# Kernel optimization log

Hardware: AMD Instinct MI355X
Metric: run time of the kernel (lower is better)

Reference implementation:

```python
import jax, jax.numpy as jnp
import numpy as np

B, T, D = 4, 2048, 2048
H, G, HD = 16, 4, 128
NB, BS = 512, 16  # num_blocks, block_size
GS = H // G
SCALE = HD ** -0.5
NEG = -1e30


def setup_inputs() -> dict:
    key = jax.random.key(0)
    ks = jax.random.split(key, 5)
    x = jax.random.normal(ks[0], (B, T, D), dtype=jnp.float32)
    block_tables = jnp.arange(B * (T // BS), dtype=jnp.int32).reshape(B, T // BS)
    kv_lens = jnp.zeros((B,), dtype=jnp.int32)
    k_blocks = jnp.zeros((NB, G, BS, HD), jnp.float32)
    v_blocks = jnp.zeros((NB, G, BS, HD), jnp.float32)
    w_q = jax.random.normal(ks[1], (D, H * HD), jnp.float32) * 0.02
    w_k = jax.random.normal(ks[2], (D, G * HD), jnp.float32) * 0.02
    w_v = jax.random.normal(ks[3], (D, G * HD), jnp.float32) * 0.02
    w_o = jax.random.normal(ks[4], (H * HD, D), jnp.float32) * 0.02
    return {"x": x, "w_q": w_q, "w_k": w_k, "w_v": w_v, "w_o": w_o,
            "k_blocks": k_blocks, "v_blocks": v_blocks,
            "block_tables": block_tables, "kv_lens": kv_lens}


def reference(x, w_q, w_k, w_v, w_o, k_blocks, v_blocks, block_tables, kv_lens):
    # projections
    q = (x @ w_q).reshape(B, T, H, HD).transpose(0, 2, 1, 3)   # [B,H,T,Hd]
    k = (x @ w_k).reshape(B, T, G, HD).transpose(0, 2, 1, 3)   # [B,G,T,Hd]
    v = (x @ w_v).reshape(B, T, G, HD).transpose(0, 2, 1, 3)

    # paged cache append (vectorized scatter over [B,T])
    pos = kv_lens[:, None] + jnp.arange(T)                     # [B,T]
    slot, off = pos // BS, pos % BS
    bid = jnp.take_along_axis(block_tables, slot, axis=1)      # [B,T] block ids
    k_blocks = k_blocks.at[bid, :, off, :].set(k.transpose(0, 2, 1, 3))
    v_blocks = v_blocks.at[bid, :, off, :].set(v.transpose(0, 2, 1, 3))

    # gather contiguous KV per request; prefill: kv_lens == 0 -> seq_len = T
    S = T
    nb = (S + BS - 1) // BS
    blk = block_tables[:, :nb]                                 # [B,nb]
    k_seq = k_blocks[blk].transpose(0, 2, 1, 3, 4).reshape(B, G, nb * BS, HD)[:, :, :S]
    v_seq = v_blocks[blk].transpose(0, 2, 1, 3, 4).reshape(B, G, nb * BS, HD)[:, :, :S]

    # original's flat reshapes pair head h with kv group (h % G)
    qg = q.reshape(B, GS, G, T, HD)
    scores = jnp.einsum('bjgqd,bgkd->bjgqk', qg, k_seq) * SCALE

    q_pos = (S - T) + jnp.arange(T)
    k_pos = jnp.arange(S)
    causal = k_pos[None, :] <= q_pos[:, None]                  # [T,S]
    scores = jnp.where(causal, scores, NEG)
    attn = jax.nn.softmax(scores, axis=-1)

    out = jnp.einsum('bjgqk,bgkd->bjgqd', attn, v_seq)         # [B,GS,G,T,Hd]
    out = out.reshape(B, H, T, HD).transpose(0, 2, 1, 3).reshape(B, T, H * HD)
    return out @ w_o
```

## Files before the change

### kernel.cpp

```cpp
#include <hip/hip_runtime.h>
#include <stdint.h>

typedef __attribute__((ext_vector_type(8))) short short8;
typedef __attribute__((ext_vector_type(8))) unsigned short ushort8;
typedef __attribute__((ext_vector_type(4))) float f32x4;

__device__ __forceinline__ ushort f2bf(float f) {
  union { float f; uint32_t u; } v; v.f = f;
  uint32_t r = v.u + 0x7FFFu + ((v.u >> 16) & 1u);
  return (ushort)(r >> 16);
}

__device__ __forceinline__ ushort f2bf_trunc(float f) {
  union { float f; uint32_t u; } v; v.f = f;
  return (ushort)(v.u >> 16);
}

__device__ __forceinline__ float fexp2(float x) {
  float r;
  asm("v_exp_f32 %0, %1" : "=v"(r) : "v"(x));
  return r;
}

__device__ __forceinline__ void gld16(const ushort* g, ushort* l) {
  __builtin_amdgcn_global_load_lds((const __attribute__((address_space(1))) void*)g,
                                   (__attribute__((address_space(3))) void*)l, 16, 0, 0);
}

__global__ __launch_bounds__(256) void k_f32_to_bf16(const float* __restrict__ in,
                                                     ushort* __restrict__ out, long n) {
  long i = ((long)blockIdx.x * 256 + threadIdx.x) * 8;
  if (i >= n) return;
  float4 a = *(const float4*)(in + i);
  float4 b = *(const float4*)(in + i + 4);
  ushort8 o;
  o[0] = f2bf(a.x); o[1] = f2bf(a.y); o[2] = f2bf(a.z); o[3] = f2bf(a.w);
  o[4] = f2bf(b.x); o[5] = f2bf(b.y); o[6] = f2bf(b.z); o[7] = f2bf(b.w);
  *(ushort8*)(out + i) = o;
}

__global__ __launch_bounds__(256) void k_w_transpose(const float* __restrict__ in,
                                                     ushort* __restrict__ out, int R, int C) {
  __shared__ float t[32][33];
  int tx = threadIdx.x & 31, ty = threadIdx.x >> 5;
  int r0 = blockIdx.y * 32, c0 = blockIdx.x * 32;
#pragma unroll
  for (int i = 0; i < 4; i++)
    t[ty + i * 8][tx] = in[(size_t)(r0 + ty + i * 8) * C + c0 + tx];
  __syncthreads();
#pragma unroll
  for (int i = 0; i < 4; i++)
    out[(size_t)(c0 + ty + i * 8) * R + r0 + tx] = f2bf(t[tx][ty + i * 8]);
}

__global__ __launch_bounds__(256) void k_v_transpose(const ushort* __restrict__ qkv,
                                                     ushort* __restrict__ out) {
  __shared__ ushort t[32][33];
  int tx = threadIdx.x & 31, ty = threadIdx.x >> 5;
  int t0 = blockIdx.x * 32, d0 = blockIdx.y * 32;
  int b = blockIdx.z >> 2, g = blockIdx.z & 3;
#pragma unroll
  for (int i = 0; i < 4; i++)
    t[ty + i * 8][tx] =
        qkv[((size_t)b * 2048 + t0 + ty + i * 8) * 3072 + 2560 + g * 128 + d0 + tx];
  __syncthreads();
#pragma unroll
  for (int i = 0; i < 4; i++)
    out[(((size_t)b * 4 + g) * 128 + d0 + ty + i * 8) * 2048 + t0 + tx] = t[tx][ty + i * 8];
}

template <int NCH8>
__device__ __forceinline__ void stageT(const ushort* G, int ldg, ushort* Ls, int tid) {
  int l = tid & 63, w = tid >> 6;
  int rsub = l >> 3;
  int cs = ((l & 7) ^ rsub) << 3;
#pragma unroll
  for (int n = 0; n < NCH8; n++) {
    int c = n * 8 + w;
    gld16(G + (size_t)(c * 8 + rsub) * ldg + cs, Ls + c * 512 + l * 8);
  }
}

template <int F32OUT, int NF>
__global__ __launch_bounds__(512) void k_gemm256(const ushort* __restrict__ A,
                                                 const ushort* __restrict__ BT,
                                                 void* __restrict__ C, int M, int N, int K) {
  constexpr int BN = NF * 64;
  __shared__ ushort As0[256 * 64], As1[256 * 64];
  __shared__ ushort Bs0[BN * 64], Bs1[BN * 64];
  const int tid = threadIdx.x;
  const int lane = tid & 63, wid = tid >> 6;
  const int wm = wid >> 2, wn = wid & 3;
  const int l15 = lane & 15, l4 = lane >> 4;
  const int rsw = (l15 & 7) << 3;
  int nwg = gridDim.x * gridDim.y;
  int lin = blockIdx.y * gridDim.x + blockIdx.x;
  int swz = (lin & 7) * (nwg >> 3) + (lin >> 3);
  int bx = swz % gridDim.x, by = swz / gridDim.x;
  const int m0 = by * 256, n0 = bx * BN;

  const ushort* Atile = A + (size_t)m0 * K;
  const ushort* Btile = BT + (size_t)n0 * K;
  const int NK = K >> 6;

  f32x4 acc[8][NF] = {};

  stageT<4>(Atile, K, As0, tid);
  stageT<NF>(Btile, K, Bs0, tid);
  stageT<4>(Atile + 64, K, As1, tid);
  stageT<NF>(Btile + 64, K, Bs1, tid);
  if constexpr (NF == 4) asm volatile("s_waitcnt vmcnt(8)" ::: "memory");
  else                   asm volatile("s_waitcnt vmcnt(7)" ::: "memory");
  asm volatile("s_barrier" ::: "memory");

  for (int kt = 0; kt < NK; ++kt) {
    const ushort* Ab = (kt & 1) ? As1 : As0;
    const ushort* Bb = (kt & 1) ? Bs1 : Bs0;
    short8 bfrag[NF][2];
#pragma unroll
    for (int nf = 0; nf < NF; nf++)
#pragma unroll
      for (int ks = 0; ks < 2; ks++)
        bfrag[nf][ks] = *(const short8*)&Bb[(wn * (NF * 16) + nf * 16 + l15) * 64 +
                                            ((ks * 32 + l4 * 8) ^ rsw)];
#pragma unroll
    for (int q = 0; q < 4; q++) {
      short8 afr[2][2];
#pragma unroll
      for (int dm = 0; dm < 2; dm++)
#pragma unroll
        for (int ks = 0; ks < 2; ks++)
          afr[dm][ks] = *(const short8*)&Ab[(wm * 128 + (q * 2 + dm) * 16 + l15) * 64 +
                                            ((ks * 32 + l4 * 8) ^ rsw)];
      __builtin_amdgcn_s_setprio(1);
#pragma unroll
      for (int dm = 0; dm < 2; dm++)
#pragma unroll
        for (int nf = 0; nf < NF; nf++)
#pragma unroll
          for (int ks = 0; ks < 2; ks++)
            acc[q * 2 + dm][nf] = __builtin_amdgcn_mfma_f32_16x16x32_bf16(
                afr[dm][ks], bfrag[nf][ks], acc[q * 2 + dm][nf], 0, 0, 0);
      __builtin_amdgcn_s_setprio(0);
    }
    asm volatile("s_barrier" ::: "memory");
    if (kt + 2 < NK) {
      stageT<4>(Atile + (kt + 2) * 64, K, (kt & 1) ? As1 : As0, tid);
      stageT<NF>(Btile + (kt + 2) * 64, K, (kt & 1) ? Bs1 : Bs0, tid);
      if constexpr (NF == 4) asm volatile("s_waitcnt vmcnt(8)" ::: "memory");
      else                   asm volatile("s_waitcnt vmcnt(7)" ::: "memory");
    } else {
      asm volatile("s_waitcnt vmcnt(0)" ::: "memory");
    }
    asm volatile("s_barrier" ::: "memory");
  }

#pragma unroll
  for (int mf = 0; mf < 8; mf++)
#pragma unroll
    for (int nf = 0; nf < NF; nf++)
#pragma unroll
      for (int r = 0; r < 4; r++) {
        int m = m0 + wm * 128 + mf * 16 + l4 * 4 + r;
        int n = n0 + wn * (NF * 16) + nf * 16 + l15;
        if (F32OUT)
          ((float*)C)[(size_t)m * N + n] = acc[mf][nf][r];
        else
          ((ushort*)C)[(size_t)m * N + n] = f2bf(acc[mf][nf][r]);
      }
}

__device__ __forceinline__ void stageA_half(const ushort* Atile, int K, int t,
                                            ushort* slot, int h, int tid) {
#pragma unroll
  for (int n = 0; n < 2; n++) {
    int row = h * 128 + n * 64 + (tid >> 3);
    int c0 = (tid & 7) * 8;
    int cs = c0 ^ ((row & 7) << 3);
    gld16(Atile + (size_t)row * K + t * 64 + cs, slot + row * 64 + c0);
  }
}

__device__ __forceinline__ void stageB_third(const ushort* Btile, int K, int t,
                                             ushort* slot, int b, int tid) {
  int row = b * 64 + (tid >> 3);
  int c0 = (tid & 7) * 8;
  int cs = c0 ^ ((row & 7) << 3);
  gld16(Btile + (size_t)row * K + t * 64 + cs, slot + row * 64 + c0);
}

__global__ __launch_bounds__(512) void k_gemm192p(const ushort* __restrict__ A,
                                                  const ushort* __restrict__ BT,
                                                  ushort* __restrict__ C, int M, int N, int K) {
  __shared__ ushort As[3][16384];
  __shared__ ushort Bs[2][12288];
  const int tid = threadIdx.x;
  const int lane = tid & 63, wid = tid >> 6;
  const int wm = wid >> 2, wn = wid & 3;
  const int l15 = lane & 15, l4 = lane >> 4;
  const int rsw = (l15 & 7) << 3;
  int nwg = gridDim.x * gridDim.y;
  int lin = blockIdx.y * gridDim.x + blockIdx.x;
  int swz = (lin & 7) * (nwg >> 3) + (lin >> 3);
  int bx = swz % gridDim.x, by = swz / gridDim.x;
  const int m0 = by * 256, n0 = bx * 192;
  const ushort* Atile = A + (size_t)m0 * K;
  const ushort* Btile = BT + (size_t)n0 * K;
  const int NK = K >> 6;

  f32x4 acc[8][3] = {};

  stageA_half(Atile, K, 0, As[0], 0, tid);
  stageA_half(Atile, K, 0, As[0], 1, tid);
  stageB_third(Btile, K, 0, Bs[0], 0, tid);
  stageB_third(Btile, K, 0, Bs[0], 1, tid);
  stageB_third(Btile, K, 0, Bs[0], 2, tid);
  stageA_half(Atile, K, 1, As[1], 0, tid);
  stageA_half(Atile, K, 1, As[1], 1, tid);
  stageB_third(Btile, K, 1, Bs[1], 0, tid);
  stageB_third(Btile, K, 1, Bs[1], 1, tid);
  stageB_third(Btile, K, 1, Bs[1], 2, tid);
  asm volatile("s_waitcnt vmcnt(7)" ::: "memory");
  asm volatile("s_barrier" ::: "memory");

#pragma unroll 1
  for (int t = 0; t < NK; ++t) {
    const ushort* Ab = As[t % 3];
    const ushort* Bb = Bs[t & 1];
    ushort* An = As[(t + 2) % 3];
    ushort* Bn = Bs[t & 1];
    const bool st = (t + 2 < NK);
    short8 bfrag[3][2];

#pragma unroll
    for (int nf = 0; nf < 3; nf++)
#pragma unroll
      for (int ks = 0; ks < 2; ks++)
        bfrag[nf][ks] = *(const short8*)&Bb[(wn * 48 + nf * 16 + l15) * 64 +
                                            ((ks * 32 + l4 * 8) ^ rsw)];
    {
      short8 afr[2][2];
#pragma unroll
      for (int dm = 0; dm < 2; dm++)
#pragma unroll
        for (int ks = 0; ks < 2; ks++)
          afr[dm][ks] = *(const short8*)&Ab[(wm * 128 + dm * 16 + l15) * 64 +
                                            ((ks * 32 + l4 * 8) ^ rsw)];
      if (st) stageA_half(Atile, K, t + 2, An, 0, tid);
      asm volatile("s_barrier" ::: "memory");
      __builtin_amdgcn_s_setprio(1);
#pragma unroll
      for (int dm = 0; dm < 2; dm++)
#pragma unroll
        for (int nf = 0; nf < 3; nf++)
#pragma unroll
          for (int ks = 0; ks < 2; ks++)
            acc[dm][nf] = __builtin_amdgcn_mfma_f32_16x16x32_bf16(
                afr[dm][ks], bfrag[nf][ks], acc[dm][nf], 0, 0, 0);
      __builtin_amdgcn_s_setprio(0);
      asm volatile("s_barrier" ::: "memory");
    }
#pragma unroll
    for (int q = 1; q < 4; q++) {
      short8 afr[2][2];
#pragma unroll
      for (int dm = 0; dm < 2; dm++)
#pragma unroll
        for (int ks = 0; ks < 2; ks++)
          afr[dm][ks] = *(const short8*)&Ab[(wm * 128 + (q * 2 + dm) * 16 + l15) * 64 +
                                            ((ks * 32 + l4 * 8) ^ rsw)];
      if (st) {
        if (q == 1) stageB_third(Btile, K, t + 2, Bn, 0, tid);
        if (q == 2) stageB_third(Btile, K, t + 2, Bn, 1, tid);
        if (q == 3) {
          stageA_half(Atile, K, t + 2, An, 1, tid);
          stageB_third(Btile, K, t + 2, Bn, 2, tid);
        }
      }
      asm volatile("s_barrier" ::: "memory");
      __builtin_amdgcn_s_setprio(1);
#pragma unroll
      for (int dm = 0; dm < 2; dm++)
#pragma unroll
        for (int nf = 0; nf < 3; nf++)
#pragma unroll
          for (int ks = 0; ks < 2; ks++)
            acc[q * 2 + dm][nf] = __builtin_amdgcn_mfma_f32_16x16x32_bf16(
                afr[dm][ks], bfrag[nf][ks], acc[q * 2 + dm][nf], 0, 0, 0);
      __builtin_amdgcn_s_setprio(0);
      if (q < 3) {
        asm volatile("s_barrier" ::: "memory");
      } else {
        if (st) asm volatile("s_waitcnt vmcnt(7)" ::: "memory");
        else    asm volatile("s_waitcnt vmcnt(0)" ::: "memory");
        asm volatile("s_barrier" ::: "memory");
      }
    }
  }

#pragma unroll
  for (int mf = 0; mf < 8; mf++)
#pragma unroll
    for (int nf = 0; nf < 3; nf++)
#pragma unroll
      for (int r = 0; r < 4; r++) {
        int m = m0 + wm * 128 + mf * 16 + l4 * 4 + r;
        int n = n0 + wn * 48 + nf * 16 + l15;
        C[(size_t)m * N + n] = f2bf(acc[mf][nf][r]);
      }
}

__device__ __forceinline__ void stage_k8(const ushort* Kt, ushort* Ks, int tid) {
  int l = tid & 63, w = tid >> 6;
#pragma unroll
  for (int n = 0; n < 2; n++) {
    int cidx = w * 2 + n;
    int r = cidx * 4 + (l >> 4);
    int cs = ((l & 15) * 8) ^ ((r & 7) << 3);
    gld16(Kt + (size_t)r * 3072 + cs, Ks + cidx * 512 + l * 8);
  }
}

__device__ __forceinline__ void stage_v8(const ushort* Vt, ushort* Vs, int tid) {
  int l = tid & 63, w = tid >> 6;
#pragma unroll
  for (int n = 0; n < 2; n++) {
    int cidx = w * 2 + n;
    int d = cidx * 8 + (l >> 3);
    int cs = ((l & 7) * 8) ^ ((d & 7) << 3);
    gld16(Vt + (size_t)d * 2048 + cs, Vs + cidx * 512 + l * 8);
  }
}

__global__ __launch_bounds__(512) void k_attn(const ushort* __restrict__ QKV,
                                              const ushort* __restrict__ VT,
                                              ushort* __restrict__ O) {
  const int T = 2048, HD = 128, G = 4, H = 16, RS = 3072;
  const float SCALE2 = 0.08838834764831845f * 1.4426950408889634f;
  const float MFIX = 12.0f;
  int bid = blockIdx.x;
  int pr = bid >> 6;
  int bh = bid & 63;
  int h = bh & 15, b = bh >> 4;
  int g = h & 3;
  int tid = threadIdx.x, wid = tid >> 6, lane = tid & 63;
  int l15 = lane & 15, l4 = lane >> 4;
  int kswz = (l15 & 7) << 3;

  __shared__ __align__(16) char smem[102400];
  ushort* Ks0 = (ushort*)smem;
  ushort* Ks1 = (ushort*)(smem + 16384);
  ushort* Vs0 = (ushort*)(smem + 32768);
  ushort* Vs1 = (ushort*)(smem + 49152);
  ushort* Pw  = (ushort*)(smem + 65536) + wid * (32 * 72);

  const ushort* Qb = &QKV[(size_t)b * T * RS + h * HD];
  const ushort* Kb = &QKV[(size_t)b * T * RS + 2048 + g * HD];
  const ushort* Vb = &VT[((size_t)b * G + g) * (size_t)HD * T];

#pragma unroll 1
  for (int half = 0; half < 2; half++) {
    int ch = half ? pr : (7 - pr);
    int qw = ch * 256 + wid * 32;
    int nt = 4 * (ch + 1);

    short8 qf[2][4];
#pragma unroll
    for (int mf = 0; mf < 2; mf++)
#pragma unroll
      for (int kf = 0; kf < 4; kf++)
        qf[mf][kf] = *(const short8*)&Qb[(size_t)(qw + mf * 16 + l15) * RS + kf * 32 + l4 * 8];

    f32x4 o[2][8] = {};
    float lrow[8];
#pragma unroll
    for (int i = 0; i < 8; i++) lrow[i] = 0.f;

    stage_k8(Kb, Ks0, tid);
    stage_v8(Vb, Vs0, tid);
    __syncthreads();

#pragma unroll 1
    for (int it = 0; it < nt; ++it) {
      int t0 = it * 64;
      int cur = it & 1;
      ushort* Kc = cur ? Ks1 : Ks0;
      ushort* Vc = cur ? Vs1 : Vs0;
      if (it + 1 < nt) {
        stage_k8(Kb + (size_t)(t0 + 64) * RS, cur ? Ks0 : Ks1, tid);
        stage_v8(Vb + t0 + 64, cur ? Vs0 : Vs1, tid);
      }
      if (t0 <= qw + 31) {
        f32x4 s[2][4] = {};
#pragma unroll
        for (int kf = 0; kf < 4; kf++) {
#pragma unroll
          for (int nf = 0; nf < 4; nf++) {
            short8 bk = *(const short8*)&Kc[(nf * 16 + l15) * 128 + ((kf * 32 + l4 * 8) ^ kswz)];
            s[0][nf] = __builtin_amdgcn_mfma_f32_16x16x32_bf16(qf[0][kf], bk, s[0][nf], 0, 0, 0);
            s[1][nf] = __builtin_amdgcn_mfma_f32_16x16x32_bf16(qf[1][kf], bk, s[1][nf], 0, 0, 0);
          }
        }
        bool needmask = (t0 + 63 > qw);
        if (needmask) {
#pragma unroll
          for (int mf = 0; mf < 2; mf++)
#pragma unroll
            for (int nf = 0; nf < 4; nf++)
#pragma unroll
              for (int r = 0; r < 4; r++) {
                int qq = qw + mf * 16 + l4 * 4 + r;
                int kk = t0 + nf * 16 + l15;
                if (kk > qq) s[mf][nf][r] = -1e30f;
              }
        }
        float rs[8];
#pragma unroll
        for (int i = 0; i < 8; i++) rs[i] = 0.f;
#pragma unroll
        for (int mf = 0; mf < 2; mf++)
#pragma unroll
          for (int nf = 0; nf < 4; nf++)
#pragma unroll
            for (int r = 0; r < 4; r++) {
              float pq = fexp2(__builtin_fmaf(s[mf][nf][r], SCALE2, -MFIX));
              rs[mf * 4 + r] += pq;
              Pw[(mf * 16 + l4 * 4 + r) * 72 + nf * 16 + l15] = f2bf_trunc(pq);
            }
#pragma unroll
        for (int i = 0; i < 8; i++) lrow[i] += rs[i];
#pragma unroll
        for (int kf = 0; kf < 2; kf++) {
          short8 pa0 = *(const short8*)&Pw[(l15) * 72 + kf * 32 + l4 * 8];
          short8 pa1 = *(const short8*)&Pw[(16 + l15) * 72 + kf * 32 + l4 * 8];
#pragma unroll
          for (int nfo = 0; nfo < 8; nfo++) {
            short8 bv = *(const short8*)&Vc[(nfo * 16 + l15) * 64 + ((kf * 32 + l4 * 8) ^ kswz)];
            o[0][nfo] = __builtin_amdgcn_mfma_f32_16x16x32_bf16(pa0, bv, o[0][nfo], 0, 0, 0);
            o[1][nfo] = __builtin_amdgcn_mfma_f32_16x16x32_bf16(pa1, bv, o[1][nfo], 0, 0, 0);
          }
        }
      }
      __syncthreads();
    }

#pragma unroll
    for (int i = 0; i < 8; i++) {
      float x = lrow[i];
      x += __shfl_xor(x, 1);
      x += __shfl_xor(x, 2);
      x += __shfl_xor(x, 4);
      x += __shfl_xor(x, 8);
      lrow[i] = x;
    }
    float inv[8];
#pragma unroll
    for (int i = 0; i < 8; i++) inv[i] = 1.0f / lrow[i];
#pragma unroll
    for (int mf = 0; mf < 2; mf++)
#pragma unroll
      for (int nfo = 0; nfo < 8; nfo++)
#pragma unroll
        for (int r = 0; r < 4; r++) {
          int t = qw + mf * 16 + l4 * 4 + r;
          int d = nfo * 16 + l15;
          O[(((size_t)b * T + t) * H + h) * HD + d] = f2bf(o[mf][nfo][r] * inv[mf * 4 + r]);
        }
    __syncthreads();
  }
}

extern "C" void kernel_launch(void* const* d_in, const int* in_sizes, int n_in,
                              void* d_out, int out_size, void* d_ws, size_t ws_size,
                              hipStream_t stream) {
  const float* x   = (const float*)d_in[0];
  const float* w_q = (const float*)d_in[1];
  const float* w_k = (const float*)d_in[2];
  const float* w_v = (const float*)d_in[3];
  const float* w_o = (const float*)d_in[4];

  char* ws = (char*)d_ws;
  ushort* xbf  = (ushort*)(ws);
  ushort* wkvT = (ushort*)(ws + 33554432ul);
  ushort* woT  = (ushort*)(ws + 46137344ul);
  ushort* qkvb = (ushort*)(ws + 54525952ul);
  ushort* VTb  = (ushort*)(ws + 104857600ul);
  ushort* attn = xbf;

  k_f32_to_bf16<<<8192, 256, 0, stream>>>(x, xbf, 16777216L);
  k_w_transpose<<<dim3(64, 64), 256, 0, stream>>>(w_q, wkvT, 2048, 2048);
  k_w_transpose<<<dim3(16, 64), 256, 0, stream>>>(w_k, wkvT + 2048ul * 2048, 2048, 512);
  k_w_transpose<<<dim3(16, 64), 256, 0, stream>>>(w_v, wkvT + 2560ul * 2048, 2048, 512);
  k_w_transpose<<<dim3(64, 64), 256, 0, stream>>>(w_o, woT, 2048, 2048);

  k_gemm192p<<<dim3(16, 32), 512, 0, stream>>>(xbf, wkvT, qkvb, 8192, 3072, 2048);

  k_v_transpose<<<dim3(64, 4, 16), 256, 0, stream>>>(qkvb, VTb);

  k_attn<<<256, 512, 0, stream>>>(qkvb, VTb, attn);

  k_gemm256<1, 4><<<dim3(8, 32), 512, 0, stream>>>(attn, woT, (float*)d_out, 8192, 2048, 2048);
}
```

Baseline: 306.4 us.

## Replace output-projection GEMM with interleaved-staging pipelined 256x256 kernel

The output projection GEMM is switched to a new kernel that triple-buffers A and double-buffers B in shared memory. Global-to-LDS loads for tile t+2 are split into pieces and issued between the four MFMA sub-phases, with barriers around each. This spreads memory traffic across the compute phases instead of issuing it all in one burst after the MFMAs. The cost is more barriers per K step and a larger LDS footprint (160KB), which may limit occupancy.

```diff
diff --git a/kernel.cpp b/kernel.cpp
--- a/kernel.cpp
+++ b/kernel.cpp
@@ -67,107 +67,6 @@
 #pragma unroll
   for (int i = 0; i < 4; i++)
     out[(((size_t)b * 4 + g) * 128 + d0 + ty + i * 8) * 2048 + t0 + tx] = t[tx][ty + i * 8];
-}
-
-template <int NCH8>
-__device__ __forceinline__ void stageT(const ushort* G, int ldg, ushort* Ls, int tid) {
-  int l = tid & 63, w = tid >> 6;
-  int rsub = l >> 3;
-  int cs = ((l & 7) ^ rsub) << 3;
-#pragma unroll
-  for (int n = 0; n < NCH8; n++) {
-    int c = n * 8 + w;
-    gld16(G + (size_t)(c * 8 + rsub) * ldg + cs, Ls + c * 512 + l * 8);
-  }
-}
-
-template <int F32OUT, int NF>
-__global__ __launch_bounds__(512) void k_gemm256(const ushort* __restrict__ A,
-                                                 const ushort* __restrict__ BT,
-                                                 void* __restrict__ C, int M, int N, int K) {
-  constexpr int BN = NF * 64;
-  __shared__ ushort As0[256 * 64], As1[256 * 64];
-  __shared__ ushort Bs0[BN * 64], Bs1[BN * 64];
-  const int tid = threadIdx.x;
-  const int lane = tid & 63, wid = tid >> 6;
-  const int wm = wid >> 2, wn = wid & 3;
-  const int l15 = lane & 15, l4 = lane >> 4;
-  const int rsw = (l15 & 7) << 3;
-  int nwg = gridDim.x * gridDim.y;
-  int lin = blockIdx.y * gridDim.x + blockIdx.x;
-  int swz = (lin & 7) * (nwg >> 3) + (lin >> 3);
-  int bx = swz % gridDim.x, by = swz / gridDim.x;
-  const int m0 = by * 256, n0 = bx * BN;
-
-  const ushort* Atile = A + (size_t)m0 * K;
-  const ushort* Btile = BT + (size_t)n0 * K;
-  const int NK = K >> 6;
-
-  f32x4 acc[8][NF] = {};
-
-  stageT<4>(Atile, K, As0, tid);
-  stageT<NF>(Btile, K, Bs0, tid);
-  stageT<4>(Atile + 64, K, As1, tid);
-  stageT<NF>(Btile + 64, K, Bs1, tid);
-  if constexpr (NF == 4) asm volatile("s_waitcnt vmcnt(8)" ::: "memory");
-  else                   asm volatile("s_waitcnt vmcnt(7)" ::: "memory");
-  asm volatile("s_barrier" ::: "memory");
-
-  for (int kt = 0; kt < NK; ++kt) {
-    const ushort* Ab = (kt & 1) ? As1 : As0;
-    const ushort* Bb = (kt & 1) ? Bs1 : Bs0;
-    short8 bfrag[NF][2];
-#pragma unroll
-    for (int nf = 0; nf < NF; nf++)
-#pragma unroll
-      for (int ks = 0; ks < 2; ks++)
-        bfrag[nf][ks] = *(const short8*)&Bb[(wn * (NF * 16) + nf * 16 + l15) * 64 +
-                                            ((ks * 32 + l4 * 8) ^ rsw)];
-#pragma unroll
-    for (int q = 0; q < 4; q++) {
-      short8 afr[2][2];
-#pragma unroll
-      for (int dm = 0; dm < 2; dm++)
-#pragma unroll
-        for (int ks = 0; ks < 2; ks++)
-          afr[dm][ks] = *(const short8*)&Ab[(wm * 128 + (q * 2 + dm) * 16 + l15) * 64 +
-                                            ((ks * 32 + l4 * 8) ^ rsw)];
-      __builtin_amdgcn_s_setprio(1);
-#pragma unroll
-      for (int dm = 0; dm < 2; dm++)
-#pragma unroll
-        for (int nf = 0; nf < NF; nf++)
-#pragma unroll
-          for (int ks = 0; ks < 2; ks++)
-            acc[q * 2 + dm][nf] = __builtin_amdgcn_mfma_f32_16x16x32_bf16(
-                afr[dm][ks], bfrag[nf][ks], acc[q * 2 + dm][nf], 0, 0, 0);
-      __builtin_amdgcn_s_setprio(0);
-    }
-    asm volatile("s_barrier" ::: "memory");
-    if (kt + 2 < NK) {
-      stageT<4>(Atile + (kt + 2) * 64, K, (kt & 1) ? As1 : As0, tid);
-      stageT<NF>(Btile + (kt + 2) * 64, K, (kt & 1) ? Bs1 : Bs0, tid);
-      if constexpr (NF == 4) asm volatile("s_waitcnt vmcnt(8)" ::: "memory");
-      else                   asm volatile("s_waitcnt vmcnt(7)" ::: "memory");
-    } else {
-      asm volatile("s_waitcnt vmcnt(0)" ::: "memory");
-    }
-    asm volatile("s_barrier" ::: "memory");
-  }
-
-#pragma unroll
-  for (int mf = 0; mf < 8; mf++)
-#pragma unroll
-    for (int nf = 0; nf < NF; nf++)
-#pragma unroll
-      for (int r = 0; r < 4; r++) {
-        int m = m0 + wm * 128 + mf * 16 + l4 * 4 + r;
-        int n = n0 + wn * (NF * 16) + nf * 16 + l15;
-        if (F32OUT)
-          ((float*)C)[(size_t)m * N + n] = acc[mf][nf][r];
-        else
-          ((ushort*)C)[(size_t)m * N + n] = f2bf(acc[mf][nf][r]);
-      }
 }
 
 __device__ __forceinline__ void stageA_half(const ushort* Atile, int K, int t,
@@ -310,6 +209,130 @@
       }
 }
 
+__global__ __launch_bounds__(512) void k_gemm256p4(const ushort* __restrict__ A,
+                                                   const ushort* __restrict__ BT,
+                                                   float* __restrict__ C, int M, int N, int K) {
+  __shared__ ushort As[3][16384];
+  __shared__ ushort Bs[2][16384];
+  const int tid = threadIdx.x;
+  const int lane = tid & 63, wid = tid >> 6;
+  const int wm = wid >> 2, wn = wid & 3;
+  const int l15 = lane & 15, l4 = lane >> 4;
+  const int rsw = (l15 & 7) << 3;
+  int nwg = gridDim.x * gridDim.y;
+  int lin = blockIdx.y * gridDim.x + blockIdx.x;
+  int swz = (lin & 7) * (nwg >> 3) + (lin >> 3);
+  int bx = swz % gridDim.x, by = swz / gridDim.x;
+  const int m0 = by * 256, n0 = bx * 256;
+  const ushort* Atile = A + (size_t)m0 * K;
+  const ushort* Btile = BT + (size_t)n0 * K;
+  const int NK = K >> 6;
+
+  f32x4 acc[8][4] = {};
+
+  stageA_half(Atile, K, 0, As[0], 0, tid);
+  stageA_half(Atile, K, 0, As[0], 1, tid);
+  stageB_third(Btile, K, 0, Bs[0], 0, tid);
+  stageB_third(Btile, K, 0, Bs[0], 1, tid);
+  stageB_third(Btile, K, 0, Bs[0], 2, tid);
+  stageB_third(Btile, K, 0, Bs[0], 3, tid);
+  stageA_half(Atile, K, 1, As[1], 0, tid);
+  stageA_half(Atile, K, 1, As[1], 1, tid);
+  stageB_third(Btile, K, 1, Bs[1], 0, tid);
+  stageB_third(Btile, K, 1, Bs[1], 1, tid);
+  stageB_third(Btile, K, 1, Bs[1], 2, tid);
+  stageB_third(Btile, K, 1, Bs[1], 3, tid);
+  asm volatile("s_waitcnt vmcnt(8)" ::: "memory");
+  asm volatile("s_barrier" ::: "memory");
+
+#pragma unroll 1
+  for (int t = 0; t < NK; ++t) {
+    const ushort* Ab = As[t % 3];
+    const ushort* Bb = Bs[t & 1];
+    ushort* An = As[(t + 2) % 3];
+    ushort* Bn = Bs[t & 1];
+    const bool st = (t + 2 < NK);
+    short8 bfrag[4][2];
+
+#pragma unroll
+    for (int nf = 0; nf < 4; nf++)
+#pragma unroll
+      for (int ks = 0; ks < 2; ks++)
+        bfrag[nf][ks] = *(const short8*)&Bb[(wn * 64 + nf * 16 + l15) * 64 +
+                                            ((ks * 32 + l4 * 8) ^ rsw)];
+    {
+      short8 afr[2][2];
+#pragma unroll
+      for (int dm = 0; dm < 2; dm++)
+#pragma unroll
+        for (int ks = 0; ks < 2; ks++)
+          afr[dm][ks] = *(const short8*)&Ab[(wm * 128 + dm * 16 + l15) * 64 +
+                                            ((ks * 32 + l4 * 8) ^ rsw)];
+      if (st) stageA_half(Atile, K, t + 2, An, 0, tid);
+      asm volatile("s_barrier" ::: "memory");
+      __builtin_amdgcn_s_setprio(1);
+#pragma unroll
+      for (int dm = 0; dm < 2; dm++)
+#pragma unroll
+        for (int nf = 0; nf < 4; nf++)
+#pragma unroll
+          for (int ks = 0; ks < 2; ks++)
+            acc[dm][nf] = __builtin_amdgcn_mfma_f32_16x16x32_bf16(
+                afr[dm][ks], bfrag[nf][ks], acc[dm][nf], 0, 0, 0);
+      __builtin_amdgcn_s_setprio(0);
+      asm volatile("s_barrier" ::: "memory");
+    }
+#pragma unroll
+    for (int q = 1; q < 4; q++) {
+      short8 afr[2][2];
+#pragma unroll
+      for (int dm = 0; dm < 2; dm++)
+#pragma unroll
+        for (int ks = 0; ks < 2; ks++)
+          afr[dm][ks] = *(const short8*)&Ab[(wm * 128 + (q * 2 + dm) * 16 + l15) * 64 +
+                                            ((ks * 32 + l4 * 8) ^ rsw)];
+      if (st) {
+        if (q == 1) stageB_third(Btile, K, t + 2, Bn, 0, tid);
+        if (q == 2) stageB_third(Btile, K, t + 2, Bn, 1, tid);
+        if (q == 3) {
+          stageA_half(Atile, K, t + 2, An, 1, tid);
+          stageB_third(Btile, K, t + 2, Bn, 2, tid);
+          stageB_third(Btile, K, t + 2, Bn, 3, tid);
+        }
+      }
+      asm volatile("s_barrier" ::: "memory");
+      __builtin_amdgcn_s_setprio(1);
+#pragma unroll
+      for (int dm = 0; dm < 2; dm++)
+#pragma unroll
+        for (int nf = 0; nf < 4; nf++)
+#pragma unroll
+          for (int ks = 0; ks < 2; ks++)
+            acc[q * 2 + dm][nf] = __builtin_amdgcn_mfma_f32_16x16x32_bf16(
+                afr[dm][ks], bfrag[nf][ks], acc[q * 2 + dm][nf], 0, 0, 0);
+      __builtin_amdgcn_s_setprio(0);
+      if (q < 3) {
+        asm volatile("s_barrier" ::: "memory");
+      } else {
+        if (st) asm volatile("s_waitcnt vmcnt(8)" ::: "memory");
+        else    asm volatile("s_waitcnt vmcnt(0)" ::: "memory");
+        asm volatile("s_barrier" ::: "memory");
+      }
+    }
+  }
+
+#pragma unroll
+  for (int mf = 0; mf < 8; mf++)
+#pragma unroll
+    for (int nf = 0; nf < 4; nf++)
+#pragma unroll
+      for (int r = 0; r < 4; r++) {
+        int m = m0 + wm * 128 + mf * 16 + l4 * 4 + r;
+        int n = n0 + wn * 64 + nf * 16 + l15;
+        C[(size_t)m * N + n] = acc[mf][nf][r];
+      }
+}
+
 __device__ __forceinline__ void stage_k8(const ushort* Kt, ushort* Ks, int tid) {
   int l = tid & 63, w = tid >> 6;
 #pragma unroll
@@ -499,5 +522,5 @@
 
   k_attn<<<256, 512, 0, stream>>>(qkvb, VTb, attn);
 
-  k_gemm256<1, 4><<<dim3(8, 32), 512, 0, stream>>>(attn, woT, (float*)d_out, 8192, 2048, 2048);
-}
+  k_gemm256p4<<<dim3(8, 32), 512, 0, stream>>>(attn, woT, (float*)d_out, 8192, 2048, 2048);
+}
```

New measurement: 300.5 us (median of 2 runs). Within noise of the previous version (-1.9%).
